# Performance work log

Hardware: AMD Instinct MI355X
Metric: run time of the kernel (lower is better)

## Reference

```python
import jax, jax.numpy as jnp
import numpy as np

N_NODES = 50000
N_EDGES = 1200000
N_REL = 40
N_BASES = 30
EMB = 64
HID = 128
N_GRAPHS = 64


def rgcn_layer(h, src, dst, edge_type, comp, basis, root, bias):
    # W_r = sum_b comp[r,b] * basis[b]  -> [R, in, out]
    W = jnp.einsum('rb,bio->rio', comp, basis)
    n = h.shape[0]
    # aggregate source features per (target node, relation): mean aggregation (PyG RGCNConv default)
    seg = dst * N_REL + edge_type                      # [E]
    msgs = h[src]                                      # [E, in]  (gather)
    agg = jax.ops.segment_sum(msgs, seg, num_segments=n * N_REL)
    agg = agg.reshape(n, N_REL, -1)                    # [N, R, in]
    cnt = jax.ops.segment_sum(jnp.ones((src.shape[0],), h.dtype), seg,
                              num_segments=n * N_REL).reshape(n, N_REL, 1)
    agg = agg / jnp.maximum(cnt, 1.0)
    out = jnp.einsum('nri,rio->no', agg, W) + h @ root + bias
    return out


def setup_inputs() -> dict:
    key = jax.random.key(0)
    ks = jax.random.split(key, 12)
    x = jnp.arange(N_NODES, dtype=jnp.int64) if jax.config.jax_enable_x64 else jnp.arange(N_NODES, dtype=jnp.int32)
    edge_index = jax.random.randint(ks[0], (2, N_EDGES), 0, N_NODES)
    edge_type = jax.random.randint(ks[1], (N_EDGES,), 0, N_REL)
    batch = jnp.sort(jax.random.randint(ks[2], (N_NODES,), 0, N_GRAPHS))
    s = 0.05
    node_emb = jax.random.normal(ks[3], (N_NODES, EMB), jnp.float32)
    comp1 = jax.random.normal(ks[4], (N_REL, N_BASES), jnp.float32) * s
    basis1 = jax.random.normal(ks[5], (N_BASES, EMB, HID), jnp.float32) * s
    root1 = jax.random.normal(ks[6], (EMB, HID), jnp.float32) * s
    bias1 = jnp.zeros((HID,), jnp.float32)
    comp2 = jax.random.normal(ks[7], (N_REL, N_BASES), jnp.float32) * s
    basis2 = jax.random.normal(ks[8], (N_BASES, HID, HID), jnp.float32) * s
    root2 = jax.random.normal(ks[9], (HID, HID), jnp.float32) * s
    bias2 = jnp.zeros((HID,), jnp.float32)
    return {"x": x, "edge_index": edge_index, "edge_type": edge_type, "batch": batch,
            "node_emb": node_emb,
            "comp1": comp1, "basis1": basis1, "root1": root1, "bias1": bias1,
            "comp2": comp2, "basis2": basis2, "root2": root2, "bias2": bias2}


def reference(x, edge_index, edge_type, batch, node_emb,
              comp1, basis1, root1, bias1, comp2, basis2, root2, bias2):
    src, dst = edge_index[0], edge_index[1]
    h = node_emb[x]                                              # embedding lookup
    h = jax.nn.relu(rgcn_layer(h, src, dst, edge_type, comp1, basis1, root1, bias1))
    h = jax.nn.relu(rgcn_layer(h, src, dst, edge_type, comp2, basis2, root2, bias2))
    # global mean pool over graphs in batch
    sums = jax.ops.segment_sum(h, batch, num_segments=N_GRAPHS)  # [G, HID]
    cnts = jax.ops.segment_sum(jnp.ones((h.shape[0],), h.dtype), batch,
                               num_segments=N_GRAPHS)[:, None]
    return sums / jnp.maximum(cnts, 1.0)
```

## Files before the change

### kernel.cpp

```cpp
#include <hip/hip_runtime.h>


#define N_NODES 50000
#define N_EDGES 1200000
#define N_REL   40
#define N_BASES 30
#define EMB     64
#define HID     128
#define N_GRAPHS 64

#define NCH     4
#define CHN     (N_NODES / NCH)
#define CAPR    312500
#define NKEYC   (NCH * N_REL)
#define PERM_CAP ((size_t)N_EDGES + (size_t)NKEYC * 256)
#define CAPB    1280

typedef float f32x4  __attribute__((ext_vector_type(4)));
typedef short bf16x8 __attribute__((ext_vector_type(8)));

__device__ __forceinline__ unsigned short f2bf(float x) {
    unsigned int u = __float_as_uint(x);
    u = (u + 0x7FFFu + ((u >> 16) & 1u)) >> 16;
    return (unsigned short)u;
}
__device__ __forceinline__ float bflo(unsigned int u) { return __uint_as_float(u << 16); }
__device__ __forceinline__ float bfhi(unsigned int u) { return __uint_as_float(u & 0xffff0000u); }

#define OFF_WF1   ((size_t)0)
#define OFF_WF2   ((size_t)163840)
#define OFF_CNT   ((size_t)491520)
#define OFF_H1    ((size_t)2491520)
#define OFF_H2    ((size_t)8891520)
#define OFF_HB1   ((size_t)15291520)
#define OFF_HB2   ((size_t)16891520)
#define OFF_CNTG  ((size_t)20091520)
#define OFF_POOL  ((size_t)20091584)
#define OFF_PSRC  ((size_t)20099776)
#define OFF_POS   ((size_t)21340736)
#define OFF_PINV  ((size_t)22581696)
#define OFF_HCR   ((size_t)23822656)
#define OFF_CCR   ((size_t)23822816)
#define OFF_POCR  ((size_t)23822976)
#define OFF_HD    ((size_t)23823168)
#define OFF_CD    ((size_t)23873168)
#define OFF_POD   ((size_t)23923168)
#define OFF_PM    ((size_t)23973184)
#define OFF_RF1   ((size_t)43973184)
#define OFF_RF2   ((size_t)43977280)

template <int IN, int KT>
__global__ void k_Wfrag(const float* __restrict__ comp, const float* __restrict__ basis,
                        unsigned short* __restrict__ Wf) {
    const int FR = IN * HID;
    int idx = blockIdx.x * blockDim.x + threadIdx.x;
    if (idx >= N_REL * FR) return;
    int r = idx / FR, F = idx - r * FR;
    int j = F & 7, lane = (F >> 3) & 63, tt = F >> 9;
    int kt = tt % KT, ct = tt / KT;
    int k = kt * 32 + (lane >> 4) * 8 + j;
    int c = ct * 16 + (lane & 15);
    float s = 0.f;
#pragma unroll
    for (int b = 0; b < N_BASES; ++b)
        s += comp[r * N_BASES + b] * basis[((size_t)b * IN + k) * HID + c];
    Wf[idx] = f2bf(s);
}

template <int IN, int KT>
__global__ void k_rootfrag(const float* __restrict__ root, unsigned short* __restrict__ rf) {
    int idx = blockIdx.x * blockDim.x + threadIdx.x;
    if (idx >= IN * HID) return;
    int j = idx & 7, lane = (idx >> 3) & 63, tt = idx >> 9;
    int kt = tt % KT, ct = tt / KT;
    int k = kt * 32 + (lane >> 4) * 8 + j;
    int c = ct * 16 + (lane & 15);
    rf[idx] = f2bf(root[k * HID + c]);
}

__global__ void k_count(const int* __restrict__ dst, const int* __restrict__ etype,
                        float* __restrict__ cnt) {
    int e = blockIdx.x * blockDim.x + threadIdx.x;
    if (e >= N_EDGES) return;
    atomicAdd(&cnt[(size_t)dst[e] * N_REL + etype[e]], 1.0f);
}

__global__ void k_deg(const float* __restrict__ cnt, int* __restrict__ hist) {
    int n = blockIdx.x * blockDim.x + threadIdx.x;
    if (n >= N_NODES) return;
    float s = 0.f;
#pragma unroll 8
    for (int r = 0; r < N_REL; ++r) s += cnt[(size_t)n * N_REL + r];
    hist[n] = (int)(s + 0.5f);
}

__global__ void k_scan_d(const int* __restrict__ hist, int* __restrict__ po) {
    __shared__ int csum[256];
    int t = threadIdx.x;
    const int CH = (N_NODES + 255) / 256;
    int k0 = t * CH, k1 = min(k0 + CH, N_NODES);
    int s = 0;
    for (int k = k0; k < k1; ++k) s += hist[k];
    csum[t] = s;
    __syncthreads();
    if (t == 0) {
        int acc = 0;
        for (int i = 0; i < 256; ++i) { int v = csum[i]; csum[i] = acc; acc += v; }
        po[N_NODES] = acc;
    }
    __syncthreads();
    int base = csum[t];
    for (int k = k0; k < k1; ++k) { po[k] = base; base += hist[k]; }
}

__global__ void k_hist_cr(const int* __restrict__ dst, const int* __restrict__ etype,
                          int* __restrict__ hist) {
    __shared__ int lh[NKEYC];
    int t = threadIdx.x;
    if (t < NKEYC) lh[t] = 0;
    __syncthreads();
    int e = blockIdx.x * blockDim.x + t;
    if (e < N_EDGES) atomicAdd(&lh[(dst[e] / CHN) * N_REL + etype[e]], 1);
    __syncthreads();
    if (t < NKEYC && lh[t]) atomicAdd(&hist[t], lh[t]);
}

__global__ void k_scan_cr(const int* __restrict__ hist, int* __restrict__ po) {
    if (threadIdx.x == 0) {
        int acc = 0;
        for (int k = 0; k < NKEYC; ++k) {
            po[k] = acc;
            acc += ((hist[k] + 255) >> 8) << 8;
        }
        po[NKEYC] = acc;
    }
}

__global__ void k_fill(int* __restrict__ ps_src, int* __restrict__ ps_os,
                       float* __restrict__ ps_inv) {
    for (size_t s = (size_t)blockIdx.x * blockDim.x + threadIdx.x; s < PERM_CAP;
         s += (size_t)gridDim.x * blockDim.x) {
        ps_src[s] = 0;
        ps_os[s] = CAPR - 1;
        ps_inv[s] = 0.f;
    }
}

#define SP_EPB 1024
__global__ void k_scatter_s(const int* __restrict__ src, const int* __restrict__ dst,
                            const int* __restrict__ etype, const float* __restrict__ cnt,
                            const int* __restrict__ po_cr, int* __restrict__ cur_cr,
                            const int* __restrict__ po_d, int* __restrict__ cur_d,
                            int* __restrict__ ps_src, int* __restrict__ ps_os,
                            float* __restrict__ ps_inv) {
    __shared__ int lh[NKEYC], sbase[NKEYC];
    int t = threadIdx.x;
    if (t < NKEYC) lh[t] = 0;
    __syncthreads();
    int e0 = blockIdx.x * SP_EPB;
    int e_[4], key_[4];
#pragma unroll
    for (int i = 0; i < 4; ++i) {
        int e = e0 + t + i * 256;
        e_[i] = e;
        if (e < N_EDGES) {
            key_[i] = (dst[e] / CHN) * N_REL + etype[e];
            atomicAdd(&lh[key_[i]], 1);
        }
    }
    __syncthreads();
    if (t < NKEYC) { if (lh[t]) sbase[t] = atomicAdd(&cur_cr[t], lh[t]); lh[t] = 0; }
    __syncthreads();
#pragma unroll
    for (int i = 0; i < 4; ++i) {
        if (e_[i] < N_EDGES) {
            int e = e_[i], key = key_[i];
            int d = dst[e], r = etype[e];
            int p = atomicAdd(&lh[key], 1);
            int slot = po_cr[key] + sbase[key] + p;
            int os_g = po_d[d] + atomicAdd(&cur_d[d], 1);
            int os_l = os_g - po_d[(d / CHN) * CHN];
            ps_src[slot] = src[e];
            ps_os[slot] = os_l;
            ps_inv[slot] = 1.0f / fmaxf(cnt[(size_t)d * N_REL + r], 1.0f);
        }
    }
}

template <int IN, int KT>
__global__ __launch_bounds__(256, 4)
void k_rootgemm(const unsigned short* __restrict__ hb_in,
                const unsigned short* __restrict__ rf,
                const float* __restrict__ bias, float* __restrict__ h) {
    __shared__ unsigned short Wl[8 * KT * 64 * 8];
    {
        const f32x4* Wg = (const f32x4*)rf;
        f32x4* Wd = (f32x4*)Wl;
        for (int kk = threadIdx.x; kk < 8 * KT * 64; kk += 256) Wd[kk] = Wg[kk];
    }
    __syncthreads();

    int l = threadIdx.x & 63, wv = threadIdx.x >> 6;
    int lrow = l & 15, lk = l >> 4;
    int nbase = blockIdx.x * 64 + wv * 16;

    int nrow = min(nbase + lrow, N_NODES - 1);
    bf16x8 a[KT];
    const unsigned short* hrow = hb_in + (size_t)nrow * IN + lk * 8;
#pragma unroll
    for (int kt = 0; kt < KT; ++kt)
        a[kt] = *(const bf16x8*)(hrow + kt * 32);

    f32x4 acc[8];
#pragma unroll
    for (int ct = 0; ct < 8; ++ct) acc[ct] = (f32x4){0.f, 0.f, 0.f, 0.f};
#pragma unroll
    for (int ct = 0; ct < 8; ++ct) {
#pragma unroll
        for (int kt = 0; kt < KT; ++kt) {
            bf16x8 bb = *(const bf16x8*)(Wl + ((ct * KT + kt) * 64 + l) * 8);
            acc[ct] = __builtin_amdgcn_mfma_f32_16x16x32_bf16(a[kt], bb, acc[ct], 0, 0, 0);
        }
    }
#pragma unroll
    for (int q = 0; q < 4; ++q) {
        int n = nbase + lk * 4 + q;
        if (n < N_NODES) {
#pragma unroll
            for (int ct = 0; ct < 8; ++ct)
                h[(size_t)n * HID + ct * 16 + lrow] = acc[ct][q] + bias[ct * 16 + lrow];
        }
    }
}

template <int IN, int KT>
__global__ __launch_bounds__(256, 4)
void k_msg(const unsigned short* __restrict__ hb_in, const int* __restrict__ ps_src,
           const int* __restrict__ ps_os, const float* __restrict__ ps_inv,
           const int* __restrict__ po_cr,
           const unsigned short* __restrict__ Wf, unsigned int* __restrict__ pm) {
    __shared__ unsigned short Wl[8 * KT * 64 * 8];
    int slot0 = po_cr[0] + blockIdx.x * 256;
    if (slot0 >= po_cr[N_REL]) return;
    int r = 0;
    while (po_cr[r + 1] <= slot0) ++r;

    {
        const f32x4* Wg = (const f32x4*)(Wf + (size_t)r * (8 * KT * 64 * 8));
        f32x4* Wd = (f32x4*)Wl;
        for (int kk = threadIdx.x; kk < 8 * KT * 64; kk += 256) Wd[kk] = Wg[kk];
    }
    __syncthreads();

    int l = threadIdx.x & 63, wv = threadIdx.x >> 6;
    int lrow = l & 15, lk = l >> 4;

    for (int t = wv; t < 16; t += 4) {
        int slot = slot0 + t * 16 + lrow;
        int sv = ps_src[slot];
        int os = ps_os[slot];
        float inv = ps_inv[slot];

        bf16x8 a[KT];
        const unsigned short* hrow = hb_in + (size_t)sv * IN + lk * 8;
#pragma unroll
        for (int kt = 0; kt < KT; ++kt)
            a[kt] = *(const bf16x8*)(hrow + kt * 32);

        f32x4 acc[8];
#pragma unroll
        for (int ct = 0; ct < 8; ++ct) acc[ct] = (f32x4){0.f, 0.f, 0.f, 0.f};
#pragma unroll
        for (int ct = 0; ct < 8; ++ct) {
#pragma unroll
            for (int kt = 0; kt < KT; ++kt) {
                bf16x8 bb = *(const bf16x8*)(Wl + ((ct * KT + kt) * 64 + l) * 8);
                acc[ct] = __builtin_amdgcn_mfma_f32_16x16x32_bf16(a[kt], bb, acc[ct], 0, 0, 0);
            }
        }
#pragma unroll
        for (int q = 0; q < 4; ++q) {
            int row = lk * 4 + q;
            int osq   = __shfl(os, row);
            float ivq = __shfl(inv, row);
            unsigned int* dp = pm + (size_t)osq * 64 + lrow;
#pragma unroll
            for (int cp = 0; cp < 4; ++cp) {
                unsigned int u = (unsigned int)f2bf(acc[2 * cp][q] * ivq)
                               | ((unsigned int)f2bf(acc[2 * cp + 1][q] * ivq) << 16);
                dp[cp * 16] = u;
            }
        }
    }
}

template <bool WRITE_HB>
__global__ __launch_bounds__(256, 8)
void k_reduce(const unsigned int* __restrict__ pm, const int* __restrict__ po_d,
              int n0chunk, float* __restrict__ h, unsigned short* __restrict__ hb_out) {
    int wv = threadIdx.x >> 6, p = threadIdx.x & 63;
    int n = n0chunk + blockIdx.x * 4 + wv;
    if (n >= n0chunk + CHN) return;
    int pmbase = po_d[n0chunk];
    int b0 = po_d[n] - pmbase;
    int cn = po_d[n + 1] - pmbase - b0;
    float lo = 0.f, hi = 0.f;
    const unsigned int* rp = pm + (size_t)b0 * 64 + p;
    int k = 0;
    for (; k + 4 <= cn; k += 4) {
        unsigned int u0 = rp[0], u1 = rp[64], u2 = rp[128], u3 = rp[192];
        rp += 256;
        lo += bflo(u0) + bflo(u1) + bflo(u2) + bflo(u3);
        hi += bfhi(u0) + bfhi(u1) + bfhi(u2) + bfhi(u3);
    }
    for (; k < cn; ++k) {
        unsigned int u = rp[0];
        rp += 64;
        lo += bflo(u); hi += bfhi(u);
    }
    int cA = (p & 15) + 32 * (p >> 4);
    float* hp = h + (size_t)n * HID;
    float vA = fmaxf(hp[cA] + lo, 0.f);
    float vB = fmaxf(hp[cA + 16] + hi, 0.f);
    hp[cA] = vA;
    hp[cA + 16] = vB;
    if (WRITE_HB) {
        hb_out[(size_t)n * HID + cA] = f2bf(vA);
        hb_out[(size_t)n * HID + cA + 16] = f2bf(vB);
    }
}

__global__ void k_cvt_emb(const float* __restrict__ emb, const int* __restrict__ x,
                          unsigned short* __restrict__ hb) {
    int idx = blockIdx.x * blockDim.x + threadIdx.x;
    if (idx >= N_NODES * (EMB / 4)) return;
    int n = idx / (EMB / 4), c4 = idx % (EMB / 4);
    int row = x[n];
    float4 v = *(const float4*)(emb + (size_t)row * EMB + c4 * 4);
    ushort4 o = {f2bf(v.x), f2bf(v.y), f2bf(v.z), f2bf(v.w)};
    *(ushort4*)(hb + (size_t)n * EMB + c4 * 4) = o;
}

__global__ void k_gcount2(const int* __restrict__ batch, float* __restrict__ cntG) {
    int g = threadIdx.x;
    if (g >= N_GRAPHS) return;
    int lo = 0, hi = N_NODES;
    while (lo < hi) { int m = (lo + hi) >> 1; if (batch[m] < g) lo = m + 1; else hi = m; }
    int lb0 = lo;
    lo = 0; hi = N_NODES;
    while (lo < hi) { int m = (lo + hi) >> 1; if (batch[m] < g + 1) lo = m + 1; else hi = m; }
    cntG[g] = (float)(lo - lb0);
}

__global__ void k_pool(const float* __restrict__ h, const int* __restrict__ batch,
                       float* __restrict__ acc) {
    const int CH = 64;
    int n0 = blockIdx.x * CH;
    int o = threadIdx.x;
    int nend = min(n0 + CH, N_NODES);
    if (n0 >= N_NODES) return;
    int curg = batch[n0];
    float run = 0.f;
    for (int n = n0; n < nend; ++n) {
        int g = batch[n];
        if (g != curg) {
            atomicAdd(&acc[(size_t)curg * HID + o], run);
            run = 0.f;
            curg = g;
        }
        run += h[(size_t)n * HID + o];
    }
    atomicAdd(&acc[(size_t)curg * HID + o], run);
}

__global__ void k_final(const float* __restrict__ acc, const float* __restrict__ cntG,
                        float* __restrict__ out) {
    int idx = blockIdx.x * blockDim.x + threadIdx.x;
    if (idx >= N_GRAPHS * HID) return;
    int g = idx >> 7;
    out[idx] = acc[idx] / fmaxf(cntG[g], 1.0f);
}

extern "C" void kernel_launch(void* const* d_in, const int* in_sizes, int n_in,
                              void* d_out, int out_size, void* d_ws, size_t ws_size,
                              hipStream_t stream) {
    const int*   x         = (const int*)d_in[0];
    const int*   edge_index= (const int*)d_in[1];
    const int*   etype     = (const int*)d_in[2];
    const int*   batch     = (const int*)d_in[3];
    const float* node_emb  = (const float*)d_in[4];
    const float* comp1     = (const float*)d_in[5];
    const float* basis1    = (const float*)d_in[6];
    const float* root1     = (const float*)d_in[7];
    const float* bias1     = (const float*)d_in[8];
    const float* comp2     = (const float*)d_in[9];
    const float* basis2    = (const float*)d_in[10];
    const float* root2     = (const float*)d_in[11];
    const float* bias2     = (const float*)d_in[12];
    float* out = (float*)d_out;

    const int* src = edge_index;
    const int* dst = edge_index + N_EDGES;

    float* ws = (float*)d_ws;
    unsigned short* Wf1 = (unsigned short*)(ws + OFF_WF1);
    unsigned short* Wf2 = (unsigned short*)(ws + OFF_WF2);
    float* cnt  = ws + OFF_CNT;
    float* h1   = ws + OFF_H1;
    float* h2   = ws + OFF_H2;
    unsigned short* hb1 = (unsigned short*)(ws + OFF_HB1);
    unsigned short* hb2 = (unsigned short*)(ws + OFF_HB2);
    float* cntG = ws + OFF_CNTG;
    float* pool = ws + OFF_POOL;
    int*   ps_src = (int*)(ws + OFF_PSRC);
    int*   ps_os  = (int*)(ws + OFF_POS);
    float* ps_inv = ws + OFF_PINV;
    int*   hist_cr = (int*)(ws + OFF_HCR);
    int*   cur_cr  = (int*)(ws + OFF_CCR);
    int*   po_cr   = (int*)(ws + OFF_POCR);
    int*   hist_d  = (int*)(ws + OFF_HD);
    int*   cur_d   = (int*)(ws + OFF_CD);
    int*   po_d    = (int*)(ws + OFF_POD);
    unsigned int* pm = (unsigned int*)(ws + OFF_PM);
    unsigned short* rf1 = (unsigned short*)(ws + OFF_RF1);
    unsigned short* rf2 = (unsigned short*)(ws + OFF_RF2);

    hipMemsetAsync(cnt, 0, (size_t)N_NODES * N_REL * sizeof(float), stream);
    hipMemsetAsync(cntG, 0, (size_t)(N_GRAPHS + N_GRAPHS * HID) * sizeof(float), stream);
    hipMemsetAsync(hist_cr, 0, 2 * NKEYC * sizeof(int), stream);
    hipMemsetAsync(cur_d, 0, N_NODES * sizeof(int), stream);

    k_count<<<(N_EDGES + 255) / 256, 256, 0, stream>>>(dst, etype, cnt);
    k_deg<<<(N_NODES + 255) / 256, 256, 0, stream>>>(cnt, hist_d);
    k_scan_d<<<1, 256, 0, stream>>>(hist_d, po_d);
    k_hist_cr<<<(N_EDGES + 255) / 256, 256, 0, stream>>>(dst, etype, hist_cr);
    k_scan_cr<<<1, 64, 0, stream>>>(hist_cr, po_cr);
    k_fill<<<2048, 256, 0, stream>>>(ps_src, ps_os, ps_inv);
    k_scatter_s<<<(N_EDGES + SP_EPB - 1) / SP_EPB, 256, 0, stream>>>(
        src, dst, etype, cnt, po_cr, cur_cr, po_d, cur_d, ps_src, ps_os, ps_inv);

    k_Wfrag<EMB, 2><<<(N_REL * EMB * HID + 255) / 256, 256, 0, stream>>>(comp1, basis1, Wf1);
    k_Wfrag<HID, 4><<<(N_REL * HID * HID + 255) / 256, 256, 0, stream>>>(comp2, basis2, Wf2);
    k_rootfrag<EMB, 2><<<(EMB * HID + 255) / 256, 256, 0, stream>>>(root1, rf1);
    k_rootfrag<HID, 4><<<(HID * HID + 255) / 256, 256, 0, stream>>>(root2, rf2);

    k_cvt_emb<<<(N_NODES * (EMB / 4) + 255) / 256, 256, 0, stream>>>(node_emb, x, hb1);
    k_rootgemm<EMB, 2><<<(N_NODES + 63) / 64, 256, 0, stream>>>(hb1, rf1, bias1, h1);
    for (int c = 0; c < NCH; ++c) {
        k_msg<EMB, 2><<<CAPB, 256, 0, stream>>>(hb1, ps_src, ps_os, ps_inv,
                                                po_cr + c * N_REL, Wf1, pm);
        k_reduce<true><<<CHN / 4, 256, 0, stream>>>(pm, po_d, c * CHN, h1, hb2);
    }

    k_rootgemm<HID, 4><<<(N_NODES + 63) / 64, 256, 0, stream>>>(hb2, rf2, bias2, h2);
    for (int c = 0; c < NCH; ++c) {
        k_msg<HID, 4><<<CAPB, 256, 0, stream>>>(hb2, ps_src, ps_os, ps_inv,
                                                po_cr + c * N_REL, Wf2, pm);
        k_reduce<false><<<CHN / 4, 256, 0, stream>>>(pm, po_d, c * CHN, h2, nullptr);
    }

    k_gcount2<<<1, 64, 0, stream>>>(batch, cntG);
    k_pool<<<(N_NODES + 63) / 64, HID, 0, stream>>>(h2, batch, pool);
    k_final<<<(N_GRAPHS * HID + 255) / 256, 256, 0, stream>>>(pool, cntG, out);
}
```

Measured before the change: 1.039 ms.

## Choose node-chunk count from workspace size and compute inverse counts in-place

Chunk count is now picked at runtime from the available workspace, using 1 or 2 chunks instead of a fixed 4 when the per-message buffer fits. This cuts the number of msg/reduce launches and the per-chunk grid tail overhead. The per-edge inverse count array is replaced by a stored destination index, and the inverse is computed once per (node, relation) in the degree kernel. The trade-off is an extra indexed gather of the inverse inside the message kernel.

```diff
diff --git a/kernel.cpp b/kernel.cpp
--- a/kernel.cpp
+++ b/kernel.cpp
@@ -9,12 +9,9 @@
 #define HID     128
 #define N_GRAPHS 64
 
-#define NCH     4
-#define CHN     (N_NODES / NCH)
-#define CAPR    312500
-#define NKEYC   (NCH * N_REL)
-#define PERM_CAP ((size_t)N_EDGES + (size_t)NKEYC * 256)
-#define CAPB    1280
+#define NKEYC_MAX 160
+#define PERM_CAP  ((size_t)N_EDGES + (size_t)NKEYC_MAX * 256)
+#define SP_EPB    1024
 
 typedef float f32x4  __attribute__((ext_vector_type(4)));
 typedef short bf16x8 __attribute__((ext_vector_type(8)));
@@ -38,16 +35,16 @@
 #define OFF_POOL  ((size_t)20091584)
 #define OFF_PSRC  ((size_t)20099776)
 #define OFF_POS   ((size_t)21340736)
-#define OFF_PINV  ((size_t)22581696)
+#define OFF_PDST  ((size_t)22581696)
 #define OFF_HCR   ((size_t)23822656)
 #define OFF_CCR   ((size_t)23822816)
 #define OFF_POCR  ((size_t)23822976)
 #define OFF_HD    ((size_t)23823168)
 #define OFF_CD    ((size_t)23873168)
 #define OFF_POD   ((size_t)23923168)
-#define OFF_PM    ((size_t)23973184)
-#define OFF_RF1   ((size_t)43973184)
-#define OFF_RF2   ((size_t)43977280)
+#define OFF_RF1   ((size_t)23973184)
+#define OFF_RF2   ((size_t)23977280)
+#define OFF_PM    ((size_t)23985472)
 
 template <int IN, int KT>
 __global__ void k_Wfrag(const float* __restrict__ comp, const float* __restrict__ basis,
@@ -85,12 +82,17 @@
     atomicAdd(&cnt[(size_t)dst[e] * N_REL + etype[e]], 1.0f);
 }
 
-__global__ void k_deg(const float* __restrict__ cnt, int* __restrict__ hist) {
+__global__ void k_deg_inv(float* __restrict__ cnt, int* __restrict__ hist) {
     int n = blockIdx.x * blockDim.x + threadIdx.x;
     if (n >= N_NODES) return;
+    float* row = cnt + (size_t)n * N_REL;
     float s = 0.f;
 #pragma unroll 8
-    for (int r = 0; r < N_REL; ++r) s += cnt[(size_t)n * N_REL + r];
+    for (int r = 0; r < N_REL; ++r) {
+        float c = row[r];
+        s += c;
+        row[r] = 1.0f / fmaxf(c, 1.0f);
+    }
     hist[n] = (int)(s + 0.5f);
 }
 
@@ -114,48 +116,47 @@
 }
 
 __global__ void k_hist_cr(const int* __restrict__ dst, const int* __restrict__ etype,
-                          int* __restrict__ hist) {
-    __shared__ int lh[NKEYC];
+                          int* __restrict__ hist, int chn, int nkeyc) {
+    __shared__ int lh[NKEYC_MAX];
     int t = threadIdx.x;
-    if (t < NKEYC) lh[t] = 0;
+    if (t < nkeyc) lh[t] = 0;
     __syncthreads();
     int e = blockIdx.x * blockDim.x + t;
-    if (e < N_EDGES) atomicAdd(&lh[(dst[e] / CHN) * N_REL + etype[e]], 1);
-    __syncthreads();
-    if (t < NKEYC && lh[t]) atomicAdd(&hist[t], lh[t]);
-}
-
-__global__ void k_scan_cr(const int* __restrict__ hist, int* __restrict__ po) {
+    if (e < N_EDGES) atomicAdd(&lh[(dst[e] / chn) * N_REL + etype[e]], 1);
+    __syncthreads();
+    if (t < nkeyc && lh[t]) atomicAdd(&hist[t], lh[t]);
+}
+
+__global__ void k_scan_cr(const int* __restrict__ hist, int* __restrict__ po, int nkeyc) {
     if (threadIdx.x == 0) {
         int acc = 0;
-        for (int k = 0; k < NKEYC; ++k) {
+        for (int k = 0; k < nkeyc; ++k) {
             po[k] = acc;
             acc += ((hist[k] + 255) >> 8) << 8;
         }
-        po[NKEYC] = acc;
+        po[nkeyc] = acc;
     }
 }
 
 __global__ void k_fill(int* __restrict__ ps_src, int* __restrict__ ps_os,
-                       float* __restrict__ ps_inv) {
+                       int* __restrict__ ps_dst, int dumprow) {
     for (size_t s = (size_t)blockIdx.x * blockDim.x + threadIdx.x; s < PERM_CAP;
          s += (size_t)gridDim.x * blockDim.x) {
         ps_src[s] = 0;
-        ps_os[s] = CAPR - 1;
-        ps_inv[s] = 0.f;
-    }
-}
-
-#define SP_EPB 1024
+        ps_os[s] = dumprow;
+        ps_dst[s] = 0;
+    }
+}
+
 __global__ void k_scatter_s(const int* __restrict__ src, const int* __restrict__ dst,
-                            const int* __restrict__ etype, const float* __restrict__ cnt,
+                            const int* __restrict__ etype,
                             const int* __restrict__ po_cr, int* __restrict__ cur_cr,
                             const int* __restrict__ po_d, int* __restrict__ cur_d,
                             int* __restrict__ ps_src, int* __restrict__ ps_os,
-                            float* __restrict__ ps_inv) {
-    __shared__ int lh[NKEYC], sbase[NKEYC];
+                            int* __restrict__ ps_dst, int chn, int nkeyc) {
+    __shared__ int lh[NKEYC_MAX], sbase[NKEYC_MAX];
     int t = threadIdx.x;
-    if (t < NKEYC) lh[t] = 0;
+    if (t < nkeyc) lh[t] = 0;
     __syncthreads();
     int e0 = blockIdx.x * SP_EPB;
     int e_[4], key_[4];
@@ -164,25 +165,25 @@
         int e = e0 + t + i * 256;
         e_[i] = e;
         if (e < N_EDGES) {
-            key_[i] = (dst[e] / CHN) * N_REL + etype[e];
+            key_[i] = (dst[e] / chn) * N_REL + etype[e];
             atomicAdd(&lh[key_[i]], 1);
         }
     }
     __syncthreads();
-    if (t < NKEYC) { if (lh[t]) sbase[t] = atomicAdd(&cur_cr[t], lh[t]); lh[t] = 0; }
+    if (t < nkeyc) { if (lh[t]) sbase[t] = atomicAdd(&cur_cr[t], lh[t]); lh[t] = 0; }
     __syncthreads();
 #pragma unroll
     for (int i = 0; i < 4; ++i) {
         if (e_[i] < N_EDGES) {
             int e = e_[i], key = key_[i];
-            int d = dst[e], r = etype[e];
+            int d = dst[e];
             int p = atomicAdd(&lh[key], 1);
             int slot = po_cr[key] + sbase[key] + p;
             int os_g = po_d[d] + atomicAdd(&cur_d[d], 1);
-            int os_l = os_g - po_d[(d / CHN) * CHN];
+            int os_l = os_g - po_d[(d / chn) * chn];
             ps_src[slot] = src[e];
             ps_os[slot] = os_l;
-            ps_inv[slot] = 1.0f / fmaxf(cnt[(size_t)d * N_REL + r], 1.0f);
+            ps_dst[slot] = d;
         }
     }
 }
@@ -236,7 +237,8 @@
 template <int IN, int KT>
 __global__ __launch_bounds__(256, 4)
 void k_msg(const unsigned short* __restrict__ hb_in, const int* __restrict__ ps_src,
-           const int* __restrict__ ps_os, const float* __restrict__ ps_inv,
+           const int* __restrict__ ps_os, const int* __restrict__ ps_dst,
+           const float* __restrict__ invc,
            const int* __restrict__ po_cr,
            const unsigned short* __restrict__ Wf, unsigned int* __restrict__ pm) {
     __shared__ unsigned short Wl[8 * KT * 64 * 8];
@@ -259,7 +261,8 @@
         int slot = slot0 + t * 16 + lrow;
         int sv = ps_src[slot];
         int os = ps_os[slot];
-        float inv = ps_inv[slot];
+        int d  = ps_dst[slot];
+        float inv = invc[(size_t)d * N_REL + r];
 
         bf16x8 a[KT];
         const unsigned short* hrow = hb_in + (size_t)sv * IN + lk * 8;
@@ -297,10 +300,11 @@
 template <bool WRITE_HB>
 __global__ __launch_bounds__(256, 8)
 void k_reduce(const unsigned int* __restrict__ pm, const int* __restrict__ po_d,
-              int n0chunk, float* __restrict__ h, unsigned short* __restrict__ hb_out) {
+              int n0chunk, int chn, float* __restrict__ h,
+              unsigned short* __restrict__ hb_out) {
     int wv = threadIdx.x >> 6, p = threadIdx.x & 63;
     int n = n0chunk + blockIdx.x * 4 + wv;
-    if (n >= n0chunk + CHN) return;
+    if (n >= n0chunk + chn) return;
     int pmbase = po_d[n0chunk];
     int b0 = po_d[n] - pmbase;
     int cn = po_d[n + 1] - pmbase - b0;
@@ -414,30 +418,39 @@
     float* pool = ws + OFF_POOL;
     int*   ps_src = (int*)(ws + OFF_PSRC);
     int*   ps_os  = (int*)(ws + OFF_POS);
-    float* ps_inv = ws + OFF_PINV;
+    int*   ps_dst = (int*)(ws + OFF_PDST);
     int*   hist_cr = (int*)(ws + OFF_HCR);
     int*   cur_cr  = (int*)(ws + OFF_CCR);
     int*   po_cr   = (int*)(ws + OFF_POCR);
     int*   hist_d  = (int*)(ws + OFF_HD);
     int*   cur_d   = (int*)(ws + OFF_CD);
     int*   po_d    = (int*)(ws + OFF_POD);
-    unsigned int* pm = (unsigned int*)(ws + OFF_PM);
     unsigned short* rf1 = (unsigned short*)(ws + OFF_RF1);
     unsigned short* rf2 = (unsigned short*)(ws + OFF_RF2);
+    unsigned int* pm = (unsigned int*)(ws + OFF_PM);
+
+    size_t ws_floats = ws_size / sizeof(float);
+    int nch = 4;
+    if (ws_floats >= OFF_PM + ((size_t)N_EDGES / 1 + 12504) * 64) nch = 1;
+    else if (ws_floats >= OFF_PM + ((size_t)N_EDGES / 2 + 12504) * 64) nch = 2;
+    int chn = N_NODES / nch;
+    int nkeyc = nch * N_REL;
+    int capr = N_EDGES / nch + 12504;
+    int gridm = (capr + 255) / 256 + N_REL;
 
     hipMemsetAsync(cnt, 0, (size_t)N_NODES * N_REL * sizeof(float), stream);
     hipMemsetAsync(cntG, 0, (size_t)(N_GRAPHS + N_GRAPHS * HID) * sizeof(float), stream);
-    hipMemsetAsync(hist_cr, 0, 2 * NKEYC * sizeof(int), stream);
+    hipMemsetAsync(hist_cr, 0, 2 * NKEYC_MAX * sizeof(int), stream);
     hipMemsetAsync(cur_d, 0, N_NODES * sizeof(int), stream);
 
     k_count<<<(N_EDGES + 255) / 256, 256, 0, stream>>>(dst, etype, cnt);
-    k_deg<<<(N_NODES + 255) / 256, 256, 0, stream>>>(cnt, hist_d);
+    k_deg_inv<<<(N_NODES + 255) / 256, 256, 0, stream>>>(cnt, hist_d);
     k_scan_d<<<1, 256, 0, stream>>>(hist_d, po_d);
-    k_hist_cr<<<(N_EDGES + 255) / 256, 256, 0, stream>>>(dst, etype, hist_cr);
-    k_scan_cr<<<1, 64, 0, stream>>>(hist_cr, po_cr);
-    k_fill<<<2048, 256, 0, stream>>>(ps_src, ps_os, ps_inv);
+    k_hist_cr<<<(N_EDGES + 255) / 256, 256, 0, stream>>>(dst, etype, hist_cr, chn, nkeyc);
+    k_scan_cr<<<1, 64, 0, stream>>>(hist_cr, po_cr, nkeyc);
+    k_fill<<<2048, 256, 0, stream>>>(ps_src, ps_os, ps_dst, capr - 1);
     k_scatter_s<<<(N_EDGES + SP_EPB - 1) / SP_EPB, 256, 0, stream>>>(
-        src, dst, etype, cnt, po_cr, cur_cr, po_d, cur_d, ps_src, ps_os, ps_inv);
+        src, dst, etype, po_cr, cur_cr, po_d, cur_d, ps_src, ps_os, ps_dst, chn, nkeyc);
 
     k_Wfrag<EMB, 2><<<(N_REL * EMB * HID + 255) / 256, 256, 0, stream>>>(comp1, basis1, Wf1);
     k_Wfrag<HID, 4><<<(N_REL * HID * HID + 255) / 256, 256, 0, stream>>>(comp2, basis2, Wf2);
@@ -446,17 +459,17 @@
 
     k_cvt_emb<<<(N_NODES * (EMB / 4) + 255) / 256, 256, 0, stream>>>(node_emb, x, hb1);
     k_rootgemm<EMB, 2><<<(N_NODES + 63) / 64, 256, 0, stream>>>(hb1, rf1, bias1, h1);
-    for (int c = 0; c < NCH; ++c) {
-        k_msg<EMB, 2><<<CAPB, 256, 0, stream>>>(hb1, ps_src, ps_os, ps_inv,
-                                                po_cr + c * N_REL, Wf1, pm);
-        k_reduce<true><<<CHN / 4, 256, 0, stream>>>(pm, po_d, c * CHN, h1, hb2);
+    for (int c = 0; c < nch; ++c) {
+        k_msg<EMB, 2><<<gridm, 256, 0, stream>>>(hb1, ps_src, ps_os, ps_dst, cnt,
+                                                 po_cr + c * N_REL, Wf1, pm);
+        k_reduce<true><<<chn / 4, 256, 0, stream>>>(pm, po_d, c * chn, chn, h1, hb2);
     }
 
     k_rootgemm<HID, 4><<<(N_NODES + 63) / 64, 256, 0, stream>>>(hb2, rf2, bias2, h2);
-    for (int c = 0; c < NCH; ++c) {
-        k_msg<HID, 4><<<CAPB, 256, 0, stream>>>(hb2, ps_src, ps_os, ps_inv,
-                                                po_cr + c * N_REL, Wf2, pm);
-        k_reduce<false><<<CHN / 4, 256, 0, stream>>>(pm, po_d, c * CHN, h2, nullptr);
+    for (int c = 0; c < nch; ++c) {
+        k_msg<HID, 4><<<gridm, 256, 0, stream>>>(hb2, ps_src, ps_os, ps_dst, cnt,
+                                                 po_cr + c * N_REL, Wf2, pm);
+        k_reduce<false><<<chn / 4, 256, 0, stream>>>(pm, po_d, c * chn, chn, h2, nullptr);
     }
 
     k_gcount2<<<1, 64, 0, stream>>>(batch, cntG);
```

New measurement: 1.031 ms. About the same (-0.8%).
